# Kernel tuning notes

Hardware: AMD Instinct MI355X
Metric: run time of the kernel (lower is better)

The kernel has to match this reference:

```python
import jax, jax.numpy as jnp
import numpy as np

P = 16          # patch size
GH = GW = 29    # grid (464/16)
N = GH * GW     # 841 tokens
E = 384         # embed dim
NH = 6          # heads
HD = E // NH    # 64
DEPTH = 8
EPS = 1e-5


def _dist_bias():
    g = jnp.linspace(0.0, 1.0, GH)
    gy, gx = jnp.meshgrid(g, g, indexing='ij')
    coords = jnp.stack([gy.ravel(), gx.ravel()], axis=-1)        # [N,2]
    d2 = ((coords[None, :, :] - coords[:, None, :]) ** 2).sum(-1)  # [N,N]
    return -d2 / d2.max()                                        # in [-1,0]


def _ln(x, g, b):
    m = x.mean(-1, keepdims=True)
    v = ((x - m) ** 2).mean(-1, keepdims=True)
    return (x - m) * jax.lax.rsqrt(v + EPS) * g + b


def _shift(x, dy, dx):
    # zero-pad shift, matching F.pad default 'constant' mode in the source
    B, C, H, W = x.shape
    if dy > 0:
        x = jnp.pad(x, ((0, 0), (0, 0), (dy, 0), (0, 0)))[:, :, :H, :]
    elif dy < 0:
        x = jnp.pad(x, ((0, 0), (0, 0), (0, -dy), (0, 0)))[:, :, -H:, :]
    if dx > 0:
        x = jnp.pad(x, ((0, 0), (0, 0), (0, 0), (dx, 0)))[:, :, :, :W]
    elif dx < 0:
        x = jnp.pad(x, ((0, 0), (0, 0), (0, 0), (0, -dx)))[:, :, :, -W:]
    return x


def _patchify(x):
    B, C, H, W = x.shape
    gh, gw = H // P, W // P
    x = x.reshape(B, C, gh, P, gw, P)
    x = x.transpose(0, 2, 4, 1, 3, 5)         # [B,gh,gw,C,p,p]
    return x.reshape(B, gh * gw, C * P * P)


def setup_inputs() -> dict:
    key = jax.random.key(0)
    ks = jax.random.split(key, 8)
    D = DEPTH
    s = 0.02
    inp = {
        'x': jax.random.normal(ks[0], (16, 3, 464, 464), jnp.float32),
        'tok_ng': jnp.ones((3840,), jnp.float32),
        'tok_nb': jnp.zeros((3840,), jnp.float32),
        'tok_w1': jax.random.normal(ks[1], (3840, 768), jnp.float32) * s,
        'tok_b1': jnp.zeros((768,), jnp.float32),
        'tok_w2': jax.random.normal(ks[2], (768, 384), jnp.float32) * s,
        'tok_b2': jnp.zeros((384,), jnp.float32),
        'ln1_g': jnp.ones((D, E), jnp.float32),
        'ln1_b': jnp.zeros((D, E), jnp.float32),
        'w_qkv': jax.random.normal(ks[3], (D, E, 3 * E), jnp.float32) * s,
        'temp': jnp.full((D, NH), np.log(HD ** -0.5), jnp.float32),
        'loc_w': jnp.full((D, NH), 0.1, jnp.float32),
        'w_proj': jax.random.normal(ks[4], (D, E, E), jnp.float32) * s,
        'b_proj': jnp.zeros((D, E), jnp.float32),
        'ls1': jnp.full((D, E), 1e-4, jnp.float32),
        'ln2_g': jnp.ones((D, E), jnp.float32),
        'ln2_b': jnp.zeros((D, E), jnp.float32),
        'ff_w1': jax.random.normal(ks[5], (D, E, 4 * E), jnp.float32) * s,
        'ff_b1': jnp.zeros((D, 4 * E), jnp.float32),
        'ff_w2': jax.random.normal(ks[6], (D, 4 * E, E), jnp.float32) * s,
        'ff_b2': jnp.zeros((D, E), jnp.float32),
        'ls2': jnp.full((D, E), 1e-4, jnp.float32),
    }
    return inp


def _forward(x, tok_ng, tok_nb, tok_w1, tok_b1, tok_w2, tok_b2,
             ln1_g, ln1_b, w_qkv, temp, loc_w, w_proj, b_proj, ls1,
             ln2_g, ln2_b, ff_w1, ff_b1, ff_w2, ff_b2, ls2):
    p2 = P // 2
    shifts = [x, _shift(x, p2, 0), _shift(x, -p2, 0), _shift(x, 0, p2), _shift(x, 0, -p2)]
    patches = jnp.concatenate([_patchify(s) for s in shifts], axis=-1)  # [B,N,3840]
    h = _ln(patches, tok_ng, tok_nb)
    h = jax.nn.gelu(h @ tok_w1 + tok_b1, approximate=False)
    h = h @ tok_w2 + tok_b2                                             # [B,N,E]

    loc = _dist_bias()                                                  # [N,N]

    def block(h, p):
        (g1, b1, wqkv, tp, lw, wp, bp, l1, g2, b2, fw1, fb1, fw2, fb2, l2) = p
        y = _ln(h, g1, b1)
        qkv = (y @ wqkv).reshape(h.shape[0], N, 3, NH, HD)
        qkv = qkv.transpose(2, 0, 3, 1, 4)                              # [3,B,H,N,hd]
        q, k, v = qkv[0], qkv[1], qkv[2]
        scale = jnp.exp(tp)[:, None, None]                              # per-head temperature
        logits = jnp.einsum('bhnd,bhmd->bhnm', q, k) * scale
        logits = logits + lw[:, None, None] * loc                       # per-head locality bias
        a = jax.nn.softmax(logits, axis=-1)
        o = jnp.einsum('bhnm,bhmd->bhnd', a, v)
        o = o.transpose(0, 2, 1, 3).reshape(h.shape[0], N, E)
        h = h + l1 * (o @ wp + bp)
        y2 = _ln(h, g2, b2)
        f = jax.nn.gelu(y2 @ fw1 + fb1, approximate=False) @ fw2 + fb2
        h = h + l2 * f
        return h, None

    params = (ln1_g, ln1_b, w_qkv, temp, loc_w, w_proj, b_proj, ls1,
              ln2_g, ln2_b, ff_w1, ff_b1, ff_w2, ff_b2, ls2)
    h, _ = jax.lax.scan(block, h, params)
    return h


def reference(x, tok_ng, tok_nb, tok_w1, tok_b1, tok_w2, tok_b2,
              ln1_g, ln1_b, w_qkv, temp, loc_w, w_proj, b_proj, ls1,
              ln2_g, ln2_b, ff_w1, ff_b1, ff_w2, ff_b2, ls2):
    return _forward(x, tok_ng, tok_nb, tok_w1, tok_b1, tok_w2, tok_b2,
                    ln1_g, ln1_b, w_qkv, temp, loc_w, w_proj, b_proj, ls1,
                    ln2_g, ln2_b, ff_w1, ff_b1, ff_w2, ff_b2, ls2)
```

## Files before the change

### kernel.cpp

```cpp
#include <hip/hip_runtime.h>
#include <math.h>

typedef __attribute__((ext_vector_type(8))) short short8;
typedef __attribute__((ext_vector_type(4))) float f32x4;
typedef unsigned short u16;

#define NTOK 841
#define GRID_H 29
#define E_ 384
#define NH_ 6
#define MROWS 13456
#define MP 13568
#define MQ 14336
#define CM 5120

__device__ __forceinline__ u16 f2bf(float f) {
  union { float f; unsigned int u; } c; c.f = f;
  unsigned int u = c.u;
  return (u16)((u + 0x7fffu + ((u >> 16) & 1u)) >> 16);
}

__device__ __forceinline__ float bf2f(u16 b) {
  union { unsigned int u; float f; } c; c.u = ((unsigned int)b) << 16; return c.f;
}

__device__ __forceinline__ float gelu_exact(float v) {
  return 0.5f * v * (1.f + erff(v * 0.70710678118654752440f));
}

__device__ __forceinline__ float fexp2(float x) {
  float r; asm("v_exp_f32 %0, %1" : "=v"(r) : "v"(x)); return r;
}

__device__ __forceinline__ int swz64(int row, int col) {
  return row * 128 + ((((col >> 3) ^ (row & 7)) << 4) | ((col & 7) << 1));
}

__global__ __launch_bounds__(256) void transpose_conv(const float* __restrict__ in,
    u16* __restrict__ out, int K, int N) {
  __shared__ float tile[32][33];
  size_t zo = (size_t)blockIdx.z * K * N;
  const float* inp = in + zo;
  u16* outp = out + zo;
  int n0 = blockIdx.x * 32, k0 = blockIdx.y * 32;
  int tx = threadIdx.x & 31, ty = threadIdx.x >> 5;
  #pragma unroll
  for (int r = ty; r < 32; r += 8) tile[r][tx] = inp[(size_t)(k0 + r) * N + n0 + tx];
  __syncthreads();
  #pragma unroll
  for (int r = ty; r < 32; r += 8) outp[(size_t)(n0 + r) * K + k0 + tx] = f2bf(tile[tx][r]);
}

__global__ __launch_bounds__(256) void patch_ln(const float* __restrict__ x,
    const float* __restrict__ g, const float* __restrict__ bsh, u16* __restrict__ out,
    int t0) {
  int t = t0 + blockIdx.x;
  int tid = threadIdx.x;
  u16* orow = out + (size_t)blockIdx.x * 3840;
  if (t >= MROWS) {
    #pragma unroll
    for (int j = 0; j < 15; ++j) orow[tid + j * 256] = 0;
    return;
  }
  int bimg = t / NTOK, n = t % NTOK;
  int gy = n / GRID_H, gx = n % GRID_H;
  float vals[15];
  float s1 = 0.f, s2 = 0.f;
  #pragma unroll
  for (int j = 0; j < 15; ++j) {
    int cout = tid + j * 256;
    int s = cout / 768, rem = cout % 768;
    int c = rem / 256, rem2 = rem % 256;
    int py = rem2 / 16, px = rem2 % 16;
    int dy = (s == 1 ? 8 : 0) - (s == 2 ? 8 : 0);
    int dx = (s == 3 ? 8 : 0) - (s == 4 ? 8 : 0);
    int Y = gy * 16 + py - dy;
    int X = gx * 16 + px - dx;
    float v = 0.f;
    if (Y >= 0 && Y < 464 && X >= 0 && X < 464)
      v = x[(((size_t)bimg * 3 + c) * 464 + Y) * 464 + X];
    vals[j] = v;
    s1 += v; s2 += v * v;
  }
  #pragma unroll
  for (int m = 1; m < 64; m <<= 1) { s1 += __shfl_xor(s1, m); s2 += __shfl_xor(s2, m); }
  __shared__ float ws1[4], ws2[4];
  int wid = tid >> 6;
  if ((tid & 63) == 0) { ws1[wid] = s1; ws2[wid] = s2; }
  __syncthreads();
  s1 = ws1[0] + ws1[1] + ws1[2] + ws1[3];
  s2 = ws2[0] + ws2[1] + ws2[2] + ws2[3];
  float mean = s1 * (1.f / 3840.f);
  float var = s2 * (1.f / 3840.f) - mean * mean;
  float rs = rsqrtf(var + 1e-5f);
  #pragma unroll
  for (int j = 0; j < 15; ++j) {
    int cout = tid + j * 256;
    orow[cout] = f2bf((vals[j] - mean) * rs * g[cout] + bsh[cout]);
  }
}

__global__ __launch_bounds__(256) void ln384(const float* __restrict__ h,
    const float* __restrict__ g, const float* __restrict__ bsh, u16* __restrict__ y) {
  int row = blockIdx.x * 4 + (threadIdx.x >> 6);
  int lane = threadIdx.x & 63;
  const float* hr = h + (size_t)row * E_;
  float v[6];
  float s1 = 0.f;
  #pragma unroll
  for (int j = 0; j < 6; ++j) { v[j] = hr[lane + j * 64]; s1 += v[j]; }
  #pragma unroll
  for (int m = 1; m < 64; m <<= 1) s1 += __shfl_xor(s1, m);
  float mean = s1 * (1.f / 384.f);
  float s2 = 0.f;
  #pragma unroll
  for (int j = 0; j < 6; ++j) { float d = v[j] - mean; s2 += d * d; }
  #pragma unroll
  for (int m = 1; m < 64; m <<= 1) s2 += __shfl_xor(s2, m);
  float rs = rsqrtf(s2 * (1.f / 384.f) + 1e-5f);
  u16* yr = y + (size_t)row * E_;
  #pragma unroll
  for (int j = 0; j < 6; ++j) {
    int c = lane + j * 64;
    yr[c] = f2bf((v[j] - mean) * rs * g[c] + bsh[c]);
  }
}

__global__ __launch_bounds__(256) void ln384p(const float* __restrict__ h,
    const float* __restrict__ g, const float* __restrict__ bsh, u16* __restrict__ yp) {
  int rowp = blockIdx.x * 4 + (threadIdx.x >> 6);
  int lane = threadIdx.x & 63;
  int bg = rowp / 896, tk = rowp - bg * 896;
  u16* yr = yp + (size_t)rowp * E_;
  if (tk >= NTOK) {
    #pragma unroll
    for (int j = 0; j < 6; ++j) yr[lane + j * 64] = 0;
    return;
  }
  const float* hr = h + (size_t)(bg * NTOK + tk) * E_;
  float v[6];
  float s1 = 0.f;
  #pragma unroll
  for (int j = 0; j < 6; ++j) { v[j] = hr[lane + j * 64]; s1 += v[j]; }
  #pragma unroll
  for (int m = 1; m < 64; m <<= 1) s1 += __shfl_xor(s1, m);
  float mean = s1 * (1.f / 384.f);
  float s2 = 0.f;
  #pragma unroll
  for (int j = 0; j < 6; ++j) { float d = v[j] - mean; s2 += d * d; }
  #pragma unroll
  for (int m = 1; m < 64; m <<= 1) s2 += __shfl_xor(s2, m);
  float rs = rsqrtf(s2 * (1.f / 384.f) + 1e-5f);
  #pragma unroll
  for (int j = 0; j < 6; ++j) {
    int c = lane + j * 64;
    yr[c] = f2bf((v[j] - mean) * rs * g[c] + bsh[c]);
  }
}

template<int EPI, int TM>
__global__ __launch_bounds__(256) void gemm_bt(
    const u16* __restrict__ A, const u16* __restrict__ BT,
    int N, int K,
    const float* __restrict__ bias, const float* __restrict__ lscale,
    float* __restrict__ resid, u16* __restrict__ outb, float* __restrict__ outf) {
  constexpr int MI = TM / 32;
  constexpr int SM1 = (TM + 128) * 64 * 2;
  constexpr int SM2 = (EPI == 1) ? TM * 136 * 2 : 0;
  constexpr int SMEM = SM1 > SM2 ? SM1 : SM2;
  __shared__ alignas(16) char smem[SMEM];
  short* As = (short*)smem;
  short* Bs = As + TM * 64;
  const int gx = gridDim.x;
  const int nwg = gx * gridDim.y;
  int L = blockIdx.x + blockIdx.y * gx;
  int q8 = nwg >> 3, r8 = nwg & 7, xcd = L & 7, pos = L >> 3;
  int L2 = (xcd < r8 ? xcd * (q8 + 1) : r8 * (q8 + 1) + (xcd - r8) * q8) + pos;
  const int m0 = (L2 / gx) * TM, n0 = (L2 % gx) * 128;
  const int tid = threadIdx.x;
  const int lane = tid & 63, wid = tid >> 6;
  const int wm = wid >> 1, wn = wid & 1;
  const int rowl = lane >> 3;
  const int colc = (((lane & 7) ^ (rowl & 7)) << 3);
  f32x4 acc[MI][4] = {};
  const int nkt = K >> 6;
  for (int kt = 0; kt < nkt; ++kt) {
    __syncthreads();
    const int k0 = kt * 64;
    #pragma unroll
    for (int i = 0; i < TM / 32; ++i) {
      int chunk = i * 4 + wid;
      const u16* ga = A + (size_t)(m0 + chunk * 8 + rowl) * K + k0 + colc;
      __builtin_amdgcn_global_load_lds((const __attribute__((address_space(1))) void*)ga,
          (__attribute__((address_space(3))) void*)(As + (chunk << 9)), 16, 0, 0);
    }
    #pragma unroll
    for (int i = 0; i < 4; ++i) {
      int chunk = i * 4 + wid;
      const u16* gb = BT + (size_t)(n0 + chunk * 8 + rowl) * K + k0 + colc;
      __builtin_amdgcn_global_load_lds((const __attribute__((address_space(1))) void*)gb,
          (__attribute__((address_space(3))) void*)(Bs + (chunk << 9)), 16, 0, 0);
    }
    __syncthreads();
    #pragma unroll
    for (int kk = 0; kk < 2; ++kk) {
      short8 a[MI], bfr[4];
      #pragma unroll
      for (int mi = 0; mi < MI; ++mi) {
        int ra = wm * (TM / 2) + mi * 16 + (lane & 15);
        a[mi] = *(const short8*)(As + ra * 64 + ((((kk << 2) | (lane >> 4)) ^ (ra & 7)) << 3));
      }
      #pragma unroll
      for (int nj = 0; nj < 4; ++nj) {
        int rb = wn * 64 + nj * 16 + (lane & 15);
        bfr[nj] = *(const short8*)(Bs + rb * 64 + ((((kk << 2) | (lane >> 4)) ^ (rb & 7)) << 3));
      }
      #pragma unroll
      for (int mi = 0; mi < MI; ++mi)
        #pragma unroll
        for (int nj = 0; nj < 4; ++nj)
          acc[mi][nj] = __builtin_amdgcn_mfma_f32_16x16x32_bf16(a[mi], bfr[nj], acc[mi][nj], 0, 0, 0);
    }
  }
  const int rrow = (lane >> 4) << 2;
  const int ccol = lane & 15;
  if (EPI == 1) {
    u16* Cs = (u16*)smem;
    __syncthreads();
    #pragma unroll
    for (int mi = 0; mi < MI; ++mi)
      #pragma unroll
      for (int nj = 0; nj < 4; ++nj) {
        int cc = wn * 64 + nj * 16 + ccol;
        float bi = bias[n0 + cc];
        #pragma unroll
        for (int r = 0; r < 4; ++r) {
          int cr = wm * (TM / 2) + mi * 16 + rrow + r;
          Cs[cr * 136 + cc] = f2bf(gelu_exact(acc[mi][nj][r] + bi));
        }
      }
    __syncthreads();
    #pragma unroll
    for (int it = 0; it < TM / 16; ++it) {
      int idx = it * 256 + tid;
      int orow = idx >> 4, c = idx & 15;
      short8 v = *(const short8*)(Cs + orow * 136 + c * 8);
      *(short8*)(outb + (size_t)(m0 + orow) * N + n0 + c * 8) = v;
    }
    return;
  }
  #pragma unroll
  for (int mi = 0; mi < MI; ++mi)
    #pragma unroll
    for (int nj = 0; nj < 4; ++nj) {
      int gn = n0 + wn * 64 + nj * 16 + ccol;
      #pragma unroll
      for (int r = 0; r < 4; ++r) {
        int gm = m0 + wm * (TM / 2) + mi * 16 + rrow + r;
        float v = acc[mi][nj][r];
        if (EPI == 2) {
          outf[(size_t)gm * N + gn] = v + bias[gn];
        } else {
          float* p = resid + (size_t)gm * N + gn;
          *p = *p + lscale[gn] * (v + bias[gn]);
        }
      }
    }
}

__global__ __launch_bounds__(256) void gemm_qkv(
    const u16* __restrict__ A, const u16* __restrict__ BT,
    u16* __restrict__ Qp, u16* __restrict__ Kp, u16* __restrict__ Vp) {
  const int K = 384, N = 1152; (void)N;
  __shared__ alignas(16) char smem[128 * 136 * 2];
  short* As = (short*)smem;
  short* Bs = As + 128 * 64;
  int L = blockIdx.x + blockIdx.y * 9;
  int L2 = (L & 7) * 126 + (L >> 3);
  const int m0 = (L2 / 9) * 128, n0 = (L2 % 9) * 128;
  const int tid = threadIdx.x;
  const int lane = tid & 63, wid = tid >> 6;
  const int wm = wid >> 1, wn = wid & 1;
  const int rowl = lane >> 3;
  const int colc = (((lane & 7) ^ (rowl & 7)) << 3);
  f32x4 acc[4][4] = {};
  for (int kt = 0; kt < 6; ++kt) {
    __syncthreads();
    const int k0 = kt * 64;
    #pragma unroll
    for (int i = 0; i < 4; ++i) {
      int chunk = i * 4 + wid;
      const u16* ga = A + (size_t)(m0 + chunk * 8 + rowl) * K + k0 + colc;
      __builtin_amdgcn_global_load_lds((const __attribute__((address_space(1))) void*)ga,
          (__attribute__((address_space(3))) void*)(As + (chunk << 9)), 16, 0, 0);
      const u16* gb = BT + (size_t)(n0 + chunk * 8 + rowl) * K + k0 + colc;
      __builtin_amdgcn_global_load_lds((const __attribute__((address_space(1))) void*)gb,
          (__attribute__((address_space(3))) void*)(Bs + (chunk << 9)), 16, 0, 0);
    }
    __syncthreads();
    #pragma unroll
    for (int kk = 0; kk < 2; ++kk) {
      short8 a[4], bfr[4];
      #pragma unroll
      for (int mi = 0; mi < 4; ++mi) {
        int ra = wm * 64 + mi * 16 + (lane & 15);
        a[mi] = *(const short8*)(As + ra * 64 + ((((kk << 2) | (lane >> 4)) ^ (ra & 7)) << 3));
      }
      #pragma unroll
      for (int nj = 0; nj < 4; ++nj) {
        int rb = wn * 64 + nj * 16 + (lane & 15);
        bfr[nj] = *(const short8*)(Bs + rb * 64 + ((((kk << 2) | (lane >> 4)) ^ (rb & 7)) << 3));
      }
      #pragma unroll
      for (int mi = 0; mi < 4; ++mi)
        #pragma unroll
        for (int nj = 0; nj < 4; ++nj)
          acc[mi][nj] = __builtin_amdgcn_mfma_f32_16x16x32_bf16(a[mi], bfr[nj], acc[mi][nj], 0, 0, 0);
    }
  }
  const int seg = n0 / 384;
  const int h0 = (n0 - seg * 384) >> 6;
  const int bg = m0 / 896;
  const int tk0 = m0 - bg * 896;
  const int rrow = (lane >> 4) << 2;
  const int ccol = lane & 15;
  u16* Cs = (u16*)smem;
  __syncthreads();
  #pragma unroll
  for (int mi = 0; mi < 4; ++mi)
    #pragma unroll
    for (int nj = 0; nj < 4; ++nj) {
      int cc = wn * 64 + nj * 16 + ccol;
      #pragma unroll
      for (int r = 0; r < 4; ++r) {
        int cr = wm * 64 + mi * 16 + rrow + r;
        u16 bv = f2bf(acc[mi][nj][r]);
        if (seg == 2) Cs[cc * 136 + cr] = bv;
        else          Cs[cr * 136 + cc] = bv;
      }
    }
  __syncthreads();
  #pragma unroll
  for (int i = 0; i < 8; ++i) {
    int idx = i * 256 + tid;
    int c = idx & 7;
    int orow = idx >> 3;
    int hs = orow >> 7;
    int rl = orow & 127;
    size_t bh = (size_t)(bg * 6 + h0 + hs);
    if (seg == 2) {
      int tile_l = rl >> 6, hd = rl & 63;
      short8 v = *(const short8*)(Cs + (hs * 64 + hd) * 136 + tile_l * 64 + c * 8);
      int tile = (tk0 >> 6) + tile_l;
      *(short8*)(Vp + bh * 57344 + tile * 4096 + hd * 64 + ((c ^ (hd & 7)) << 3)) = v;
    } else {
      short8 v = *(const short8*)(Cs + rl * 136 + hs * 64 + c * 8);
      if (seg == 0) {
        *(short8*)(Qp + (bh * 896 + tk0 + rl) * 64 + c * 8) = v;
      } else {
        int tok = tk0 + rl;
        *(short8*)(Kp + bh * 57344 + (tok >> 6) * 4096 + (tok & 63) * 64 + ((c ^ (tok & 7)) << 3)) = v;
      }
    }
  }
}

__global__ __launch_bounds__(256) void attn_sk(const u16* __restrict__ Qp,
    const u16* __restrict__ Kp, const u16* __restrict__ Vp,
    const float* __restrict__ temp_d, const float* __restrict__ locw_d,
    u16* __restrict__ op, float* __restrict__ ml) {
  int Lw = blockIdx.x + 14 * blockIdx.z + 28 * blockIdx.y;
  int L2 = (Lw & 7) * 336 + (Lw >> 3);
  const int bh = L2 / 28;
  const int rem = L2 % 28;
  const int ks = rem / 14, qt = rem % 14;
  const int hh = bh % NH_;
  const int tid = threadIdx.x, lane = tid & 63, w = tid >> 6;
  const int lg = lane >> 4, lc = lane & 15;
  const float LOG2E = 1.44269504088896f;
  const float scale = __expf(temp_d[hh]) * LOG2E;
  const float lwh = locw_d[hh] * LOG2E * -0.5f;
  const int kb0 = ks * 448;

  __shared__ alignas(16) char ktl[64 * 128];
  __shared__ alignas(16) char vtl[64 * 128];
  __shared__ alignas(16) char pl[4][16 * 128];
  __shared__ float yx2[896 * 2];

  for (int j = tid; j < 896; j += 256) {
    unsigned jc = j < NTOK ? (unsigned)j : (NTOK - 1);
    yx2[j * 2]     = (float)(jc / 29u) * (1.f / 28.f);
    yx2[j * 2 + 1] = (float)(jc % 29u) * (1.f / 28.f);
  }

  const char* qb = (const char*)(Qp + ((size_t)bh * 896 + qt * 64) * 64);
  short8 qf0 = *(const short8*)(qb + (w * 16 + lc) * 128 + lg * 16);
  short8 qf1 = *(const short8*)(qb + (w * 16 + lc) * 128 + 64 + lg * 16);

  const char* kbase = (const char*)Kp + ((size_t)bh * 14 + ks * 7) * 8192;
  const char* vbase = (const char*)Vp + ((size_t)bh * 14 + ks * 7) * 8192;

  auto stage = [&](int kt) {
    #pragma unroll
    for (int i = 0; i < 2; ++i) {
      int off = (i * 4 + w) * 1024;
      __builtin_amdgcn_global_load_lds(
          (const __attribute__((address_space(1))) void*)(kbase + kt * 8192 + off + lane * 16),
          (__attribute__((address_space(3))) void*)(ktl + off), 16, 0, 0);
      __builtin_amdgcn_global_load_lds(
          (const __attribute__((address_space(1))) void*)(vbase + kt * 8192 + off + lane * 16),
          (__attribute__((address_space(3))) void*)(vtl + off), 16, 0, 0);
    }
  };

  f32x4 of[4] = {};
  float mrow[4], psum[4];
  #pragma unroll
  for (int r = 0; r < 4; ++r) { mrow[r] = -3e38f; psum[r] = 0.f; }

  stage(0);
  __syncthreads();

  float qy[4], qx[4];
  #pragma unroll
  for (int r = 0; r < 4; ++r) {
    int iq = qt * 64 + w * 16 + (lg << 2) + r;
    qy[r] = yx2[iq * 2];
    qx[r] = yx2[iq * 2 + 1];
  }

  for (int kt = 0; kt < 7; ++kt) {
    f32x4 sf[4];
    __builtin_amdgcn_s_setprio(1);
    #pragma unroll
    for (int nt = 0; nt < 4; ++nt) {
      short8 kf0 = *(const short8*)(ktl + swz64(nt * 16 + lc, lg << 3));
      short8 kf1 = *(const short8*)(ktl + swz64(nt * 16 + lc, 32 + (lg << 3)));
      f32x4 z = {0.f, 0.f, 0.f, 0.f};
      z = __builtin_amdgcn_mfma_f32_16x16x32_bf16(qf0, kf0, z, 0, 0, 0);
      z = __builtin_amdgcn_mfma_f32_16x16x32_bf16(qf1, kf1, z, 0, 0, 0);
      sf[nt] = z;
    }
    __builtin_amdgcn_s_setprio(0);

    #pragma unroll
    for (int nt = 0; nt < 4; ++nt) {
      int j = kb0 + kt * 64 + nt * 16 + lc;
      float jy = yx2[j * 2], jx = yx2[j * 2 + 1];
      #pragma unroll
      for (int r = 0; r < 4; ++r) {
        float dy = qy[r] - jy, dx = qx[r] - jx;
        float val = sf[nt][r] * scale + lwh * (dy * dy + dx * dx);
        sf[nt][r] = (j < NTOK) ? val : -3e38f;
      }
    }

    float lm[4];
    #pragma unroll
    for (int r = 0; r < 4; ++r)
      lm[r] = fmaxf(fmaxf(sf[0][r], sf[1][r]), fmaxf(sf[2][r], sf[3][r]));
    bool trig = (lm[0] > mrow[0] + 12.f) | (lm[1] > mrow[1] + 12.f) |
                (lm[2] > mrow[2] + 12.f) | (lm[3] > mrow[3] + 12.f);
    if (__any(trig)) {
      #pragma unroll
      for (int r = 0; r < 4; ++r) {
        float tm = lm[r];
        #pragma unroll
        for (int m = 1; m < 16; m <<= 1) tm = fmaxf(tm, __shfl_xor(tm, m));
        float mnew = fmaxf(mrow[r], tm);
        float alpha = fexp2(mrow[r] - mnew);
        psum[r] *= alpha;
        of[0][r] *= alpha; of[1][r] *= alpha; of[2][r] *= alpha; of[3][r] *= alpha;
        mrow[r] = mnew;
      }
    }

    char* plw = pl[w];
    #pragma unroll
    for (int nt = 0; nt < 4; ++nt)
      #pragma unroll
      for (int r = 0; r < 4; ++r) {
        float p = fexp2(sf[nt][r] - mrow[r]);
        psum[r] += p;
        *(u16*)(plw + swz64((lg << 2) + r, nt * 16 + lc)) = f2bf(p);
      }
    asm volatile("s_waitcnt lgkmcnt(0)" ::: "memory");
    __builtin_amdgcn_sched_barrier(0);
    short8 pa[2];
    #pragma unroll
    for (int t = 0; t < 2; ++t)
      pa[t] = *(const short8*)(plw + swz64(lc, t * 32 + (lg << 3)));

    __builtin_amdgcn_s_setprio(1);
    #pragma unroll
    for (int n2 = 0; n2 < 4; ++n2) {
      f32x4 accv = of[n2];
      #pragma unroll
      for (int t = 0; t < 2; ++t) {
        short8 vf = *(const short8*)(vtl + swz64(n2 * 16 + lc, t * 32 + (lg << 3)));
        accv = __builtin_amdgcn_mfma_f32_16x16x32_bf16(pa[t], vf, accv, 0, 0, 0);
      }
      of[n2] = accv;
    }
    __builtin_amdgcn_s_setprio(0);

    if (kt < 6) {
      __syncthreads();
      stage(kt + 1);
      __syncthreads();
    }
  }

  #pragma unroll
  for (int r = 0; r < 4; ++r) {
    float s = psum[r];
    #pragma unroll
    for (int m = 1; m < 16; m <<= 1) s += __shfl_xor(s, m);
    int iq = qt * 64 + w * 16 + (lg << 2) + r;
    if (iq < NTOK) {
      size_t rb = (size_t)(ks * 96 + bh) * 896 + iq;
      #pragma unroll
      for (int n2 = 0; n2 < 4; ++n2)
        op[rb * 64 + n2 * 16 + lc] = f2bf(of[n2][r]);
      if (lc == 0) { ml[rb * 2] = mrow[r]; ml[rb * 2 + 1] = s; }
    }
  }
}

__global__ __launch_bounds__(256) void combine(const u16* __restrict__ op,
    const float* __restrict__ ml, u16* __restrict__ ob) {
  const int bh = blockIdx.y, bimg = bh / NH_, hh = bh % NH_;
  const int wid = threadIdx.x >> 6, lane = threadIdx.x & 63;
  const int tokb = blockIdx.x * 16 + wid * 4;
  #pragma unroll
  for (int rr = 0; rr < 4; ++rr) {
    int tok = tokb + rr;
    if (tok >= NTOK) return;
    size_t i1 = (size_t)bh * 896 + tok;
    size_t i2 = (size_t)(96 + bh) * 896 + tok;
    float m1 = ml[i1 * 2], l1 = ml[i1 * 2 + 1];
    float m2 = ml[i2 * 2], l2 = ml[i2 * 2 + 1];
    float m = fmaxf(m1, m2);
    float w1 = fexp2(m1 - m), w2 = fexp2(m2 - m);
    float inv = 1.f / (l1 * w1 + l2 * w2);
    float o1 = bf2f(op[i1 * 64 + lane]);
    float o2 = bf2f(op[i2 * 64 + lane]);
    ob[((size_t)(bimg * NTOK + tok)) * E_ + hh * 64 + lane] =
        f2bf((o1 * w1 + o2 * w2) * inv);
  }
}

__global__ __launch_bounds__(256) void copy_out(const float* __restrict__ h, float* __restrict__ out) {
  size_t i = (size_t)blockIdx.x * 256 + threadIdx.x;
  if (i < (size_t)MROWS * E_) out[i] = h[i];
}

extern "C" void kernel_launch(void* const* d_in, const int* in_sizes, int n_in,
                              void* d_out, int out_size, void* d_ws, size_t ws_size,
                              hipStream_t stream) {
  const float* x      = (const float*)d_in[0];
  const float* tok_ng = (const float*)d_in[1];
  const float* tok_nb = (const float*)d_in[2];
  const float* tok_w1 = (const float*)d_in[3];
  const float* tok_b1 = (const float*)d_in[4];
  const float* tok_w2 = (const float*)d_in[5];
  const float* tok_b2 = (const float*)d_in[6];
  const float* ln1_g  = (const float*)d_in[7];
  const float* ln1_b  = (const float*)d_in[8];
  const float* w_qkv  = (const float*)d_in[9];
  const float* temp   = (const float*)d_in[10];
  const float* loc_w  = (const float*)d_in[11];
  const float* w_proj = (const float*)d_in[12];
  const float* b_proj = (const float*)d_in[13];
  const float* ls1    = (const float*)d_in[14];
  const float* ln2_g  = (const float*)d_in[15];
  const float* ln2_b  = (const float*)d_in[16];
  const float* ff_w1  = (const float*)d_in[17];
  const float* ff_b1  = (const float*)d_in[18];
  const float* ff_w2  = (const float*)d_in[19];
  const float* ff_b2  = (const float*)d_in[20];
  const float* ls2    = (const float*)d_in[21];
  float* out = (float*)d_out;

  char* ws = (char*)d_ws;
  size_t off = 0;
  auto alloc = [&](size_t bytes) -> void* {
    void* p = ws + off; off += (bytes + 255) & ~(size_t)255; return p;
  };
  u16* w1T   = (u16*)alloc(768UL * 3840 * 2);
  u16* w2T   = (u16*)alloc(384UL * 768 * 2);
  u16* qkvT  = (u16*)alloc(8UL * 1152 * 384 * 2);
  u16* projT = (u16*)alloc(8UL * 384 * 384 * 2);
  u16* f1T   = (u16*)alloc(8UL * 1536 * 384 * 2);
  u16* f2T   = (u16*)alloc(8UL * 384 * 1536 * 2);
  float* h   = (float*)alloc((size_t)MP * 384 * 4);
  char* regB = (char*)alloc(22500000);
  u16* h1   = (u16*)regB;
  u16* ypad = (u16*)regB;
  u16* yff  = (u16*)regB;
  u16* ob   = (u16*)(regB + 11010048);
  char* regA = (char*)alloc((size_t)MP * 1536 * 2);
  u16* Xlnc = (u16*)regA;
  u16* Qp   = (u16*)regA;
  u16* Kp   = (u16*)(regA + 11010048);
  u16* Vp   = (u16*)(regA + 22020096);
  u16* f1b  = (u16*)regA;
  u16* op   = (u16*)alloc(2UL * 96 * 896 * 64 * 2);
  float* ml = (float*)alloc(2UL * 96 * 896 * 2 * 4);
  (void)in_sizes; (void)n_in; (void)out_size;

  if (off > ws_size) return;

  transpose_conv<<<dim3(24, 120, 1), 256, 0, stream>>>(tok_w1, w1T, 3840, 768);
  transpose_conv<<<dim3(12, 24, 1), 256, 0, stream>>>(tok_w2, w2T, 768, 384);
  transpose_conv<<<dim3(36, 12, 8), 256, 0, stream>>>(w_qkv, qkvT, 384, 1152);
  transpose_conv<<<dim3(12, 12, 8), 256, 0, stream>>>(w_proj, projT, 384, 384);
  transpose_conv<<<dim3(48, 12, 8), 256, 0, stream>>>(ff_w1, f1T, 384, 1536);
  transpose_conv<<<dim3(12, 48, 8), 256, 0, stream>>>(ff_w2, f2T, 1536, 384);

  for (int m = 0; m < MP; m += CM) {
    int rows = MP - m; if (rows > CM) rows = CM;
    patch_ln<<<rows, 256, 0, stream>>>(x, tok_ng, tok_nb, Xlnc, m);
    gemm_bt<1, 128><<<dim3(6, rows / 128), 256, 0, stream>>>(Xlnc, w1T, 768, 3840,
        tok_b1, nullptr, nullptr, h1 + (size_t)m * 768, nullptr);
  }
  gemm_bt<2, 64><<<dim3(3, MP / 64), 256, 0, stream>>>(h1, w2T, 384, 768, tok_b2,
      nullptr, nullptr, nullptr, h);

  for (int d = 0; d < 8; ++d) {
    ln384p<<<MQ / 4, 256, 0, stream>>>(h, ln1_g + d * E_, ln1_b + d * E_, ypad);
    gemm_qkv<<<dim3(9, 112), 256, 0, stream>>>(ypad, qkvT + (size_t)d * 1152 * 384, Qp, Kp, Vp);
    attn_sk<<<dim3(14, 96, 2), 256, 0, stream>>>(Qp, Kp, Vp, temp + d * NH_, loc_w + d * NH_, op, ml);
    combine<<<dim3(53, 96), 256, 0, stream>>>(op, ml, ob);
    gemm_bt<3, 64><<<dim3(3, MP / 64), 256, 0, stream>>>(ob, projT + (size_t)d * 384 * 384,
        384, 384, b_proj + d * E_, ls1 + d * E_, h, nullptr, nullptr);
    ln384<<<MP / 4, 256, 0, stream>>>(h, ln2_g + d * E_, ln2_b + d * E_, yff);
    gemm_bt<1, 128><<<dim3(12, MP / 128), 256, 0, stream>>>(yff, f1T + (size_t)d * 1536 * 384,
        1536, 384, ff_b1 + d * 1536, nullptr, nullptr, f1b, nullptr);
    gemm_bt<3, 64><<<dim3(3, MP / 64), 256, 0, stream>>>(f1b, f2T + (size_t)d * 384 * 1536,
        384, 1536, ff_b2 + d * E_, ls2 + d * E_, h, nullptr, nullptr);
  }

  copy_out<<<(MROWS * E_ + 255) / 256, 256, 0, stream>>>(h, out);
}
```

Measured before the change: 1.950 ms.

## Double-buffer LDS tiles in GEMM kernels to overlap global loads with MFMA

Converts the gemm_bt and gemm_qkv main loops to use two LDS buffers. The next K-tile is issued via global_load_lds while the current tile is consumed, with explicit vmcnt waits and raw s_barriers replacing the two __syncthreads per iteration. This is meant to hide global-memory latency behind matrix math. The cost is doubled LDS footprint, which may reduce occupancy, plus reliance on hand-tuned vmcnt counts and barrier ordering for correctness; the epilogue now reuses the larger buffer.

New measurement: 1.912 ms. No clear change (-1.9%).

```diff
diff --git a/kernel.cpp b/kernel.cpp
--- a/kernel.cpp
+++ b/kernel.cpp
@@ -165,12 +165,9 @@
     const float* __restrict__ bias, const float* __restrict__ lscale,
     float* __restrict__ resid, u16* __restrict__ outb, float* __restrict__ outf) {
   constexpr int MI = TM / 32;
-  constexpr int SM1 = (TM + 128) * 64 * 2;
-  constexpr int SM2 = (EPI == 1) ? TM * 136 * 2 : 0;
-  constexpr int SMEM = SM1 > SM2 ? SM1 : SM2;
-  __shared__ alignas(16) char smem[SMEM];
+  constexpr int BUF = (TM + 128) * 64;
+  __shared__ alignas(16) char smem[2 * BUF * 2];
   short* As = (short*)smem;
-  short* Bs = As + TM * 64;
   const int gx = gridDim.x;
   const int nwg = gx * gridDim.y;
   int L = blockIdx.x + blockIdx.y * gx;
@@ -184,36 +181,53 @@
   const int colc = (((lane & 7) ^ (rowl & 7)) << 3);
   f32x4 acc[MI][4] = {};
   const int nkt = K >> 6;
-  for (int kt = 0; kt < nkt; ++kt) {
-    __syncthreads();
+
+  auto stage = [&](int b, int kt) {
+    short* Ab = As + b * BUF;
+    short* Bb = Ab + TM * 64;
     const int k0 = kt * 64;
     #pragma unroll
     for (int i = 0; i < TM / 32; ++i) {
       int chunk = i * 4 + wid;
       const u16* ga = A + (size_t)(m0 + chunk * 8 + rowl) * K + k0 + colc;
       __builtin_amdgcn_global_load_lds((const __attribute__((address_space(1))) void*)ga,
-          (__attribute__((address_space(3))) void*)(As + (chunk << 9)), 16, 0, 0);
+          (__attribute__((address_space(3))) void*)(Ab + (chunk << 9)), 16, 0, 0);
     }
     #pragma unroll
     for (int i = 0; i < 4; ++i) {
       int chunk = i * 4 + wid;
       const u16* gb = BT + (size_t)(n0 + chunk * 8 + rowl) * K + k0 + colc;
       __builtin_amdgcn_global_load_lds((const __attribute__((address_space(1))) void*)gb,
-          (__attribute__((address_space(3))) void*)(Bs + (chunk << 9)), 16, 0, 0);
-    }
-    __syncthreads();
+          (__attribute__((address_space(3))) void*)(Bb + (chunk << 9)), 16, 0, 0);
+    }
+  };
+
+  stage(0, 0);
+  for (int kt = 0; kt < nkt; ++kt) {
+    const int cur = kt & 1;
+    if (kt + 1 < nkt) {
+      stage(cur ^ 1, kt + 1);
+      if (TM == 128) asm volatile("s_waitcnt vmcnt(8)" ::: "memory");
+      else           asm volatile("s_waitcnt vmcnt(6)" ::: "memory");
+    } else {
+      asm volatile("s_waitcnt vmcnt(0)" ::: "memory");
+    }
+    __builtin_amdgcn_s_barrier();
+    __builtin_amdgcn_sched_barrier(0);
+    short* Ab = As + cur * BUF;
+    short* Bb = Ab + TM * 64;
     #pragma unroll
     for (int kk = 0; kk < 2; ++kk) {
       short8 a[MI], bfr[4];
       #pragma unroll
       for (int mi = 0; mi < MI; ++mi) {
         int ra = wm * (TM / 2) + mi * 16 + (lane & 15);
-        a[mi] = *(const short8*)(As + ra * 64 + ((((kk << 2) | (lane >> 4)) ^ (ra & 7)) << 3));
+        a[mi] = *(const short8*)(Ab + ra * 64 + ((((kk << 2) | (lane >> 4)) ^ (ra & 7)) << 3));
       }
       #pragma unroll
       for (int nj = 0; nj < 4; ++nj) {
         int rb = wn * 64 + nj * 16 + (lane & 15);
-        bfr[nj] = *(const short8*)(Bs + rb * 64 + ((((kk << 2) | (lane >> 4)) ^ (rb & 7)) << 3));
+        bfr[nj] = *(const short8*)(Bb + rb * 64 + ((((kk << 2) | (lane >> 4)) ^ (rb & 7)) << 3));
       }
       #pragma unroll
       for (int mi = 0; mi < MI; ++mi)
@@ -221,6 +235,7 @@
         for (int nj = 0; nj < 4; ++nj)
           acc[mi][nj] = __builtin_amdgcn_mfma_f32_16x16x32_bf16(a[mi], bfr[nj], acc[mi][nj], 0, 0, 0);
     }
+    __builtin_amdgcn_s_barrier();
   }
   const int rrow = (lane >> 4) << 2;
   const int ccol = lane & 15;
@@ -271,10 +286,10 @@
 __global__ __launch_bounds__(256) void gemm_qkv(
     const u16* __restrict__ A, const u16* __restrict__ BT,
     u16* __restrict__ Qp, u16* __restrict__ Kp, u16* __restrict__ Vp) {
-  const int K = 384, N = 1152; (void)N;
-  __shared__ alignas(16) char smem[128 * 136 * 2];
+  const int K = 384;
+  constexpr int BUF = 256 * 64;
+  __shared__ alignas(16) char smem[2 * BUF * 2];
   short* As = (short*)smem;
-  short* Bs = As + 128 * 64;
   int L = blockIdx.x + blockIdx.y * 9;
   int L2 = (L & 7) * 126 + (L >> 3);
   const int m0 = (L2 / 9) * 128, n0 = (L2 % 9) * 128;
@@ -284,32 +299,48 @@
   const int rowl = lane >> 3;
   const int colc = (((lane & 7) ^ (rowl & 7)) << 3);
   f32x4 acc[4][4] = {};
-  for (int kt = 0; kt < 6; ++kt) {
-    __syncthreads();
+
+  auto stage = [&](int b, int kt) {
+    short* Ab = As + b * BUF;
+    short* Bb = Ab + 128 * 64;
     const int k0 = kt * 64;
     #pragma unroll
     for (int i = 0; i < 4; ++i) {
       int chunk = i * 4 + wid;
       const u16* ga = A + (size_t)(m0 + chunk * 8 + rowl) * K + k0 + colc;
       __builtin_amdgcn_global_load_lds((const __attribute__((address_space(1))) void*)ga,
-          (__attribute__((address_space(3))) void*)(As + (chunk << 9)), 16, 0, 0);
+          (__attribute__((address_space(3))) void*)(Ab + (chunk << 9)), 16, 0, 0);
       const u16* gb = BT + (size_t)(n0 + chunk * 8 + rowl) * K + k0 + colc;
       __builtin_amdgcn_global_load_lds((const __attribute__((address_space(1))) void*)gb,
-          (__attribute__((address_space(3))) void*)(Bs + (chunk << 9)), 16, 0, 0);
-    }
-    __syncthreads();
+          (__attribute__((address_space(3))) void*)(Bb + (chunk << 9)), 16, 0, 0);
+    }
+  };
+
+  stage(0, 0);
+  for (int kt = 0; kt < 6; ++kt) {
+    const int cur = kt & 1;
+    if (kt + 1 < 6) {
+      stage(cur ^ 1, kt + 1);
+      asm volatile("s_waitcnt vmcnt(8)" ::: "memory");
+    } else {
+      asm volatile("s_waitcnt vmcnt(0)" ::: "memory");
+    }
+    __builtin_amdgcn_s_barrier();
+    __builtin_amdgcn_sched_barrier(0);
+    short* Ab = As + cur * BUF;
+    short* Bb = Ab + 128 * 64;
     #pragma unroll
     for (int kk = 0; kk < 2; ++kk) {
       short8 a[4], bfr[4];
       #pragma unroll
       for (int mi = 0; mi < 4; ++mi) {
         int ra = wm * 64 + mi * 16 + (lane & 15);
-        a[mi] = *(const short8*)(As + ra * 64 + ((((kk << 2) | (lane >> 4)) ^ (ra & 7)) << 3));
+        a[mi] = *(const short8*)(Ab + ra * 64 + ((((kk << 2) | (lane >> 4)) ^ (ra & 7)) << 3));
       }
       #pragma unroll
       for (int nj = 0; nj < 4; ++nj) {
         int rb = wn * 64 + nj * 16 + (lane & 15);
-        bfr[nj] = *(const short8*)(Bs + rb * 64 + ((((kk << 2) | (lane >> 4)) ^ (rb & 7)) << 3));
+        bfr[nj] = *(const short8*)(Bb + rb * 64 + ((((kk << 2) | (lane >> 4)) ^ (rb & 7)) << 3));
       }
       #pragma unroll
       for (int mi = 0; mi < 4; ++mi)
@@ -317,6 +348,7 @@
         for (int nj = 0; nj < 4; ++nj)
           acc[mi][nj] = __builtin_amdgcn_mfma_f32_16x16x32_bf16(a[mi], bfr[nj], acc[mi][nj], 0, 0, 0);
     }
+    __builtin_amdgcn_s_barrier();
   }
   const int seg = n0 / 384;
   const int h0 = (n0 - seg * 384) >> 6;
```
